# Performance work log

Measured on AMD Instinct MI355X. Metric: run time of the kernel, lower is better.

The kernel has to match this reference:

```python
import jax, jax.numpy as jnp
import numpy as np

BLOCK = 64      # block_size
NRAND = 3       # num_random_blocks
NUM_HEAD = 16
HEAD_DIM = 64
HIDDEN = 1024
PEN = -10000.0  # HF attn_mask_penalty


def _sparse_attn(q, k, v, band_mask, from_mask, to_mask, blocked_mask, rand_attn):
    # q,k,v: [B,H,S,D]; BigBird block-sparse attention (HF math).
    B, H, S, D = q.shape
    b, r = BLOCK, NRAND
    n = S // b
    rsd = 1.0 / (D ** 0.5)

    bq = q.reshape(B, H, n, b, D)
    bk = k.reshape(B, H, n, b, D)
    bv = v.reshape(B, H, n, b, D)

    bi = jnp.arange(B)[:, None, None, None]
    hi = jnp.arange(H)[None, :, None, None]
    # gathered random key/value blocks: [B,H,n-2,r*b,D]
    gk = bk[bi, hi, rand_attn].reshape(B, H, n - 2, r * b, D)
    gv = bv[bi, hi, rand_attn].reshape(B, H, n - 2, r * b, D)
    # random-block mask: [B,H,n-2,b,r*b]
    rm = blocked_mask[bi, rand_attn].reshape(B, H, n - 2, r * b)
    rand_mask = jnp.einsum("blq,bhlk->bhlqk", blocked_mask[:, 1:-1], rm)

    ones = lambda shp: jnp.ones(shp, q.dtype)

    # ---- first query block: attends to everything ----
    p = jnp.einsum("bhqd,bhkd->bhqk", bq[:, :, 0], k) * rsd + (1.0 - to_mask) * PEN
    c0 = jnp.einsum("bhqk,bhkd->bhqd", jax.nn.softmax(p, -1), v)[:, :, None]

    # ---- second query block: blocks 0,1,2,last + random ----
    k1 = jnp.concatenate([bk[:, :, 0], bk[:, :, 1], bk[:, :, 2], bk[:, :, -1], gk[:, :, 0]], axis=2)
    v1 = jnp.concatenate([bv[:, :, 0], bv[:, :, 1], bv[:, :, 2], bv[:, :, -1], gv[:, :, 0]], axis=2)
    p = jnp.einsum("bhqd,bhkd->bhqk", bq[:, :, 1], k1) * rsd
    seq_pad = jnp.concatenate([to_mask[..., :3 * b], to_mask[..., -b:], ones((B, 1, 1, r * b))], axis=3)
    rand_pad = jnp.concatenate([ones((B, H, b, 4 * b)), rand_mask[:, :, 0]], axis=3)
    p = p + (1.0 - jnp.minimum(seq_pad, rand_pad)) * PEN
    c1 = jnp.einsum("bhqk,bhkd->bhqd", jax.nn.softmax(p, -1), v1)[:, :, None]

    # ---- middle blocks 2..n-3: band(3 blocks) + first + last + random ----
    ek = jnp.concatenate([bk[:, :, 1:-3], bk[:, :, 2:-2], bk[:, :, 3:-1]], axis=3)  # [B,H,n-4,3b,D]
    ev = jnp.concatenate([bv[:, :, 1:-3], bv[:, :, 2:-2], bv[:, :, 3:-1]], axis=3)
    mq = bq[:, :, 2:-2]                                                              # [B,H,n-4,b,D]
    inner = jnp.einsum("bhlqd,bhlkd->bhlqk", mq, ek) * rsd + (1.0 - band_mask) * PEN
    randp = jnp.einsum("bhlqd,bhlkd->bhlqk", mq, gk[:, :, 1:-1]) * rsd + (1.0 - rand_mask[:, :, 1:-1]) * PEN
    firstp = jnp.einsum("bhlqd,bhkd->bhlqk", mq, bk[:, :, 0]) * rsd + (1.0 - to_mask[..., :b][:, :, None]) * PEN
    lastp = jnp.einsum("bhlqd,bhkd->bhlqk", mq, bk[:, :, -1]) * rsd + (1.0 - to_mask[..., -b:][:, :, None]) * PEN
    band = jnp.concatenate([firstp, inner, randp, lastp], axis=-1)  # [B,H,n-4,b,(5+r)*b]
    a = jax.nn.softmax(band, -1)
    cm = jnp.einsum("bhlqk,bhlkd->bhlqd", a[..., b:4 * b], ev)
    cm = cm + jnp.einsum("bhlqk,bhlkd->bhlqd", a[..., 4 * b:-b], gv[:, :, 1:-1])
    cm = cm + jnp.einsum("bhlqk,bhkd->bhlqd", a[..., :b], bv[:, :, 0])
    cm = cm + jnp.einsum("bhlqk,bhkd->bhlqd", a[..., -b:], bv[:, :, -1])

    # ---- second-last query block: blocks 0,-3,-2,-1 + random ----
    k2 = jnp.concatenate([bk[:, :, 0], bk[:, :, -3], bk[:, :, -2], bk[:, :, -1], gk[:, :, -1]], axis=2)
    v2 = jnp.concatenate([bv[:, :, 0], bv[:, :, -3], bv[:, :, -2], bv[:, :, -1], gv[:, :, -1]], axis=2)
    p = jnp.einsum("bhqd,bhkd->bhqk", bq[:, :, -2], k2) * rsd
    seq_pad = jnp.concatenate([to_mask[..., :b], to_mask[..., -3 * b:], ones((B, 1, 1, r * b))], axis=3)
    rand_pad = jnp.concatenate([ones((B, H, b, 4 * b)), rand_mask[:, :, -1]], axis=3)
    p = p + (1.0 - jnp.minimum(seq_pad, rand_pad)) * PEN
    c2 = jnp.einsum("bhqk,bhkd->bhqd", jax.nn.softmax(p, -1), v2)[:, :, None]

    # ---- last query block: attends to everything ----
    p = jnp.einsum("bhqd,bhkd->bhqk", bq[:, :, -1], k) * rsd + (1.0 - to_mask) * PEN
    c3 = jnp.einsum("bhqk,bhkd->bhqd", jax.nn.softmax(p, -1), v)[:, :, None]

    ctx = jnp.concatenate([c0, c1, cm, c2, c3], axis=2).reshape(B, H, S, D)
    ctx = ctx * from_mask  # [B,1,S,1]
    return ctx.transpose(0, 2, 1, 3).reshape(B, S, H * D)


def setup_inputs() -> dict:
    key = jax.random.key(0)
    ks = jax.random.split(key, 12)
    B, L = 2, 4064
    S = 4096
    n = S // BLOCK
    sc = 0.02
    inp = {
        "X": jax.random.normal(ks[0], (B, L, HIDDEN), jnp.float32),
        "Wq": jax.random.normal(ks[1], (HIDDEN, NUM_HEAD * HEAD_DIM), jnp.float32) * sc,
        "b_q": jnp.zeros((NUM_HEAD * HEAD_DIM,), jnp.float32),
        "Wk": jax.random.normal(ks[2], (HIDDEN, NUM_HEAD * HEAD_DIM), jnp.float32) * sc,
        "b_k": jnp.zeros((NUM_HEAD * HEAD_DIM,), jnp.float32),
        "Wv": jax.random.normal(ks[3], (HIDDEN, NUM_HEAD * HEAD_DIM), jnp.float32) * sc,
        "b_v": jnp.zeros((NUM_HEAD * HEAD_DIM,), jnp.float32),
        "Wo": jax.random.normal(ks[4], (NUM_HEAD * HEAD_DIM, HIDDEN), jnp.float32) * sc,
        "b_o": jnp.zeros((HIDDEN,), jnp.float32),
        "band_mask": jnp.ones((B, 1, n - 4, BLOCK, 3 * BLOCK), jnp.float32),
        "from_mask": jnp.ones((B, 1, S, 1), jnp.float32),
        "to_mask": jnp.ones((B, 1, 1, S), jnp.float32),
        "blocked_encoder_mask": jnp.ones((B, n, BLOCK), jnp.float32),
        "rand_attn": jax.random.randint(ks[5], (B, NUM_HEAD, n - 2, NRAND), 0, n, jnp.int32),
    }
    return inp


def reference(X, Wq, b_q, Wk, b_k, Wv, b_v, Wo, b_o,
              band_mask, from_mask, to_mask, blocked_encoder_mask, rand_attn):
    B, L, _ = X.shape
    pad = BLOCK - L % BLOCK  # matches torch wrapper (pads full block if L % b == 0)
    Xp = jnp.pad(X, ((0, 0), (0, pad), (0, 0)))
    S = L + pad

    def proj(W, bias):
        return (Xp @ W + bias).reshape(B, S, NUM_HEAD, HEAD_DIM).transpose(0, 2, 1, 3)

    q, k, v = proj(Wq, b_q), proj(Wk, b_k), proj(Wv, b_v)
    attn = _sparse_attn(q, k, v, band_mask, from_mask, to_mask, blocked_encoder_mask, rand_attn)
    out = attn @ Wo + b_o
    return out[:, :L]
```

## Files before the change

### kernel.cpp

```cpp
#include <hip/hip_runtime.h>

#define BB 2
#define SEQ 4096
#define LQ 4064
#define HID 1024
#define NH 16
#define HD 64
#define NB 64
#define BLK 64
#define NR 3
#define PENV -10000.0f

typedef __bf16 bf16;
typedef __bf16 bf16x8 __attribute__((ext_vector_type(8)));
typedef float floatx4 __attribute__((ext_vector_type(4)));

__device__ inline floatx4 mfma16(bf16x8 a, bf16x8 b, floatx4 c) {
    return __builtin_amdgcn_mfma_f32_16x16x32_bf16(a, b, c, 0, 0, 0);
}

__device__ inline void async_ld16(const bf16* g, bf16* l) {
    __builtin_amdgcn_global_load_lds(
        (const __attribute__((address_space(1))) unsigned int*)g,
        (__attribute__((address_space(3))) unsigned int*)l, 16, 0, 0);
}

__global__ __launch_bounds__(256) void cast_pad_x(const float* __restrict__ X,
                                                  bf16* __restrict__ Xp) {
    int t = blockIdx.x * 256 + threadIdx.x;
    int c4 = t & 255;
    int row = t >> 8;
    int b = row >> 12;
    int s = row & 4095;
    float4 v = make_float4(0.f, 0.f, 0.f, 0.f);
    if (s < LQ) {
        v = reinterpret_cast<const float4*>(X + ((size_t)(b * LQ + s)) * HID)[c4];
    }
    union { bf16 h[4]; uint2 u; } o;
    o.h[0] = (bf16)v.x; o.h[1] = (bf16)v.y; o.h[2] = (bf16)v.z; o.h[3] = (bf16)v.w;
    *reinterpret_cast<uint2*>(Xp + (size_t)row * HID + c4 * 4) = o.u;
}

__global__ __launch_bounds__(256) void transpose_w(const float* __restrict__ Wq,
                                                   const float* __restrict__ Wk,
                                                   const float* __restrict__ Wv,
                                                   const float* __restrict__ Wo,
                                                   bf16* __restrict__ WqkvT,
                                                   bf16* __restrict__ WoT) {
    __shared__ float tile[64][65];
    int sel = blockIdx.z;
    const float* src = (sel == 0) ? Wq : (sel == 1) ? Wk : (sel == 2) ? Wv : Wo;
    bf16* dst = (sel < 3) ? (WqkvT + (size_t)sel * HID * HID) : WoT;
    int j0 = blockIdx.x * 64, k0 = blockIdx.y * 64;
    int tx = threadIdx.x, ty = threadIdx.y;
    for (int i = 0; i < 16; i++) {
        int k = ty + i * 4;
        tile[k][tx] = src[(size_t)(k0 + k) * HID + j0 + tx];
    }
    __syncthreads();
    for (int i = 0; i < 16; i++) {
        int j = ty + i * 4;
        dst[(size_t)(j0 + j) * HID + k0 + tx] = (bf16)tile[tx][j];
    }
}

__global__ __launch_bounds__(256) void transpose_band(const float* __restrict__ band,
                                                      float* __restrict__ bandT) {
    __shared__ float tile[64][65];
    int kt = blockIdx.x;
    int lrow = blockIdx.y;
    int b = blockIdx.z;
    const float* src = band + ((size_t)(b * (NB - 4) + lrow) * BLK) * 192;
    float* dst = bandT + ((size_t)(b * (NB - 4) + lrow) * 192) * BLK;
    int tx = threadIdx.x, ty = threadIdx.y;
    for (int i = 0; i < 16; i++) {
        int qq = i * 4 + ty;
        tile[qq][tx] = src[(size_t)qq * 192 + kt * 64 + tx];
    }
    __syncthreads();
    for (int i = 0; i < 16; i++) {
        int k = i * 4 + ty;
        dst[(size_t)(kt * 64 + k) * BLK + tx] = tile[tx][k];
    }
}

__global__ __launch_bounds__(256) void mask_viol(const float* __restrict__ tom,
                                                 const float* __restrict__ blocked,
                                                 const float* __restrict__ band,
                                                 int* __restrict__ flags) {
    int which = blockIdx.y, b = blockIdx.z;
    const float* src;
    size_t n;
    if (which == 0)      { src = tom     + (size_t)b * SEQ;                  n = SEQ; }
    else if (which == 1) { src = blocked + (size_t)b * NB * BLK;             n = NB * BLK; }
    else                 { src = band    + (size_t)b * (NB - 4) * BLK * 192; n = (size_t)(NB - 4) * BLK * 192; }
    const float4* s4 = (const float4*)src;
    size_t n4 = n >> 2;
    int bad = 0;
    for (size_t i = blockIdx.x * 256 + threadIdx.x; i < n4; i += 240 * 256) {
        float4 v = s4[i];
        bad |= (v.x != 1.0f) | (v.y != 1.0f) | (v.z != 1.0f) | (v.w != 1.0f);
    }
    if (__any(bad) && (threadIdx.x & 63) == 0)
        atomicOr(&flags[which * BB + b], 1);
}

__global__ __launch_bounds__(256) void gemm_qkv(const bf16* __restrict__ Xp,
// ... 10 lines not shown
    int tid = threadIdx.x;
    int wave = tid >> 6, lane = tid & 63;
    int quad = lane >> 4, lm = lane & 15;
    int id = blockIdx.x;
    int xcd = id & 7, slot = id >> 3;
    int tile_m = (xcd * 8 + (slot & 7)) * 128;
    int tile_n = (slot >> 3) * 128;
    int wm = (wave & 1) * 64, wn = (wave >> 1) * 64;

    floatx4 acc[4][4] = {};

    for (int k0 = 0; k0 < HID; k0 += 64) {
        __syncthreads();
        for (int it = 0; it < 4; it++) {
            int c = it * 256 + tid;
            int row = c >> 3, col = (c & 7) * 8;
            async_ld16(Xp + (size_t)(tile_m + row) * HID + k0 + col, &As[c * 8]);
            async_ld16(WT + (size_t)(tile_n + row) * HID + k0 + col, &Bs[c * 8]);
        }
        __syncthreads();
        for (int ks = 0; ks < 64; ks += 32) {
            bf16x8 a[4], b[4];
            for (int i = 0; i < 4; i++)
                a[i] = *reinterpret_cast<const bf16x8*>(&As[(wm + i * 16 + lm) * 64 + ks + quad * 8]);
            for (int j = 0; j < 4; j++)
                b[j] = *reinterpret_cast<const bf16x8*>(&Bs[(wn + j * 16 + lm) * 64 + ks + quad * 8]);
            for (int i = 0; i < 4; i++)
                for (int j = 0; j < 4; j++)
                    acc[i][j] = mfma16(a[i], b[j], acc[i][j]);
        }
    }

    int which = tile_n >> 10;
    int hc_base = (tile_n + wn) & 1023;
    int h = hc_base >> 6;
    const float* bias = (which == 0) ? bq : (which == 1) ? bk : bv;
    __syncthreads();
    bf16* ep = (bf16*)smem + wave * (64 * 72);

    if (which < 2) {
        #pragma unroll
        for (int i = 0; i < 4; i++)
            #pragma unroll
            for (int j = 0; j < 4; j++) {
                float bsv = bias[hc_base + j * 16 + lm];
                #pragma unroll
                for (int r = 0; r < 4; r++) {
                    float val = acc[i][j][r] + bsv;
                    if (which == 0) val *= 0.125f;
                    ep[(i * 16 + quad * 4 + r) * 72 + j * 16 + lm] = (bf16)val;
                }
            }
        __builtin_amdgcn_wave_barrier();
        int s_glob = tile_m + wm + lane;
        int b_ = s_glob >> 12, s = s_glob & 4095;
        bf16* dstb = ((which == 0) ? qo : ko) + ((size_t)((b_ * NH + h) * SEQ + s)) * HD;
        #pragma unroll
        for (int c = 0; c < 8; c++)
            *reinterpret_cast<uint4*>(dstb + c * 8) =
                *reinterpret_cast<const uint4*>(ep + lane * 72 + c * 8);
    } else {
        #pragma unroll
        for (int i = 0; i < 4; i++)
            #pragma unroll
            for (int j = 0; j < 4; j++) {
                float bsv = bias[hc_base + j * 16 + lm];
                #pragma unroll
                for (int r = 0; r < 4; r++) {
                    float val = acc[i][j][r] + bsv;
                    ep[(j * 16 + lm) * 72 + i * 16 + quad * 4 + r] = (bf16)val;
                }
            }
        __builtin_amdgcn_wave_barrier();
        int s_base = tile_m + wm;
        int b_ = s_base >> 12, s0 = s_base & 4095;
        bf16* dstb = vt + ((size_t)((b_ * NH + h) * HD + lane)) * SEQ + s0;
        #pragma unroll
        for (int c = 0; c < 8; c++)
            *reinterpret_cast<uint4*>(dstb + c * 8) =
                *reinterpret_cast<const uint4*>(ep + lane * 72 + c * 8);
    }
}

__global__ __launch_bounds__(256, 3) void attn_kernel(const bf16* __restrict__ q,
                                                      const bf16* __restrict__ kk,
                                                      const bf16* __restrict__ vt,
                                                      const float* __restrict__ bandT,
                                                      const float* __restrict__ fromm,
                                                      const float* __restrict__ tom,
                                                      const float* __restrict__ blocked,
                                                      const int* __restrict__ rand_attn,
                                                      const int* __restrict__ flags,
                                                      bf16* __restrict__ attn) {
    __shared__ __align__(16) char smem[17408];

    int tid = threadIdx.x, wave = tid >> 6, lane = tid & 63;
    int quad = lane >> 4, lm = lane & 15;
    int bh = blockIdx.x;
    int b = bh >> 4, h = bh & 15;
    size_t bh_base = (size_t)bh * SEQ * HD;
    int x = blockIdx.y;
    bool fullmode = (x < 8);
    int l, sub;
    if (fullmode) { l = (x >> 2) ? (NB - 1) : 0; sub = x & 3; }
    else          { l = x - 7;                   sub = wave;  }

    bool do_to = flags[b] != 0;
    bool do_bl = flags[BB + b] != 0;
    bool do_bd = flags[2 * BB + b] != 0;

    bf16x8 aq0 = *reinterpret_cast<const bf16x8*>(
        q + bh_base + (size_t)(l * BLK + sub * 16 + lm) * HD + quad * 8);
    bf16x8 aq1 = *reinterpret_cast<const bf16x8*>(
        q + bh_base + (size_t)(l * BLK + sub * 16 + lm) * HD + 32 + quad * 8);

    floatx4 ctx[4] = {};
    float mrun = -1e30f, lrun = 0.f;
    float mq = blocked[((size_t)b * NB + l) * BLK + sub * 16 + lm];

    unsigned long long kbp = 0ull;
    unsigned int typ_p = 0u;
    if (!fullmode) {
        int base;
        if (l == 1) {
            kbp = (1ull << 8) | (2ull << 16) | ((unsigned long long)(NB - 1) << 24);
            base = 4;
        } else if (l == NB - 2) {
            kbp = ((unsigned long long)(NB - 3) << 8) | ((unsigned long long)(NB - 2) << 16) |
                  ((unsigned long long)(NB - 1) << 24);
            base = 4;
        } else {
            kbp = ((unsigned long long)(l - 1) << 8) | ((unsigned long long)l << 16) |
                  ((unsigned long long)(l + 1) << 24) | ((unsigned long long)(NB - 1) << 32);
            typ_p = (1u << 4) | (2u << 8) | (3u << 12);
            base = 5;
        }
        const int* ra = rand_attn + ((size_t)(b * NH + h) * (NB - 2) + (l - 1)) * NR;
        #pragma unroll
        for (int r = 0; r < NR; r++) {
            int rv = __builtin_amdgcn_readfirstlane(ra[r]);
            kbp   |= (unsigned long long)(rv & 63) << ((base + r) * 8);
            typ_p |= 4u << ((base + r) * 4);
        }
        for (int i = base + NR; i < 8; i++) typ_p |= 5u << (i * 4);
    }

    bf16* pw = (bf16*)smem + wave * 16 * 136;

    int nch = fullmode ? 8 : 4;
    for (int ch = 0; ch < nch; ch++) {
        int i0 = ch * 2, i1 = i0 + 1;
        int kb0, kb1, ty0, ty1;
        if (fullmode) {
            kb0 = __builtin_amdgcn_readfirstlane(wave * 16 + i0);
            kb1 = kb0 + 1;
            ty0 = 0; ty1 = 0;
        } else {
            kb0 = __builtin_amdgcn_readfirstlane((int)((kbp >> (i0 * 8)) & 63));
            kb1 = __builtin_amdgcn_readfirstlane((int)((kbp >> (i1 * 8)) & 63));
            ty0 = (int)((typ_p >> (i0 * 4)) & 15);
            ty1 = (int)((typ_p >> (i1 * 4)) & 15);
        }

        const bf16* k0p = kk + bh_base + (size_t)kb0 * (BLK * HD);
        const bf16* k1p = kk + bh_base + (size_t)kb1 * (BLK * HD);
        bf16x8 kfa[2][4], kfb[2][4];
        #pragma unroll
        for (int f = 0; f < 4; f++) {
            kfa[0][f] = *reinterpret_cast<const bf16x8*>(k0p + (f * 16 + lm) * HD + quad * 8);
            kfb[0][f] = *reinterpret_cast<const bf16x8*>(k0p + (f * 16 + lm) * HD + 32 + quad * 8);
        }
        #pragma unroll
        for (int f = 0; f < 4; f++) {
            kfa[1][f] = *reinterpret_cast<const bf16x8*>(k1p + (f * 16 + lm) * HD + quad * 8);
            kfb[1][f] = *reinterpret_cast<const bf16x8*>(k1p + (f * 16 + lm) * HD + 32 + quad * 8);
        }

        floatx4 sc[2][4];
        #pragma unroll
        for (int u = 0; u < 2; u++)
            #pragma unroll
            for (int f = 0; f < 4; f++) {
                floatx4 z = {0.f, 0.f, 0.f, 0.f};
                z = mfma16(kfa[u][f], aq0, z);
                z = mfma16(kfb[u][f], aq1, z);
                sc[u][f] = z;
            }

        const bf16* v0p = vt + bh_base + (size_t)kb0 * BLK;
        bf16x8 vf0[4][2];
        #pragma unroll
        for (int dj = 0; dj < 4; dj++) {
            vf0[dj][0] = *reinterpret_cast<const bf16x8*>(v0p + (size_t)(dj * 16 + lm) * SEQ + quad * 8);
            vf0[dj][1] = *reinterpret_cast<const bf16x8*>(v0p + (size_t)(dj * 16 + lm) * SEQ + 32 + quad * 8);
        }

        {
            int kbs[2] = {kb0, kb1};
            int tys[2] = {ty0, ty1};
            #pragma unroll
            for (int u = 0; u < 2; u++) {
                int kb = kbs[u], typ = tys[u];
                if (typ == 0) {
                    if (do_to) {
                        #pragma unroll
                        for (int f = 0; f < 4; f++) {
                            float4 t4 = *reinterpret_cast<const float4*>(
                                tom + (size_t)b * SEQ + kb * BLK + f * 16 + quad * 4);
                            sc[u][f][0] += (1.f - t4.x) * PENV;
                            sc[u][f][1] += (1.f - t4.y) * PENV;
                            sc[u][f][2] += (1.f - t4.z) * PENV;
                            sc[u][f][3] += (1.f - t4.w) * PENV;
                        }
                    }
                } else if (typ == 4) {
                    if (do_bl) {
                        #pragma unroll
                        for (int f = 0; f < 4; f++) {
                            float4 t4 = *reinterpret_cast<const float4*>(
                                blocked + ((size_t)b * NB + kb) * BLK + f * 16 + quad * 4);
                            sc[u][f][0] += (1.f - mq * t4.x) * PENV;
                            sc[u][f][1] += (1.f - mq * t4.y) * PENV;
                            sc[u][f][2] += (1.f - mq * t4.z) * PENV;
                            sc[u][f][3] += (1.f - mq * t4.w) * PENV;
                        }
                    }
                } else if (typ != 5) {
                    if (do_bd) {
                        int t = typ - 1;
                        const float* bp = bandT + ((size_t)(b * (NB - 4) + (l - 2)) * 192 + t * 64) * BLK;
                        #pragma unroll
                        for (int f = 0; f < 4; f++)
                            #pragma unroll
                            for (int r = 0; r < 4; r++) {
                                float bm = bp[(size_t)(f * 16 + quad * 4 + r) * BLK + sub * 16 + lm];
                                sc[u][f][r] += (1.f - bm) * PENV;
                            }
                    }
                } else {
                    #pragma unroll
                    for (int f = 0; f < 4; f++)
                        #pragma unroll
                        for (int r = 0; r < 4; r++) sc[u][f][r] += PENV;
                }
            }
        }

        float mx = -1e30f;
        #pragma unroll
        for (int u = 0; u < 2; u++)
            #pragma unroll
            for (int f = 0; f < 4; f++)
                #pragma unroll
                for (int r = 0; r < 4; r++) mx = fmaxf(mx, sc[u][f][r]);
        mx = fmaxf(mx, __shfl_xor(mx, 16, 64));
        mx = fmaxf(mx, __shfl_xor(mx, 32, 64));
        float mnew = fmaxf(mrun, mx);
        float scale = __expf(mrun - mnew);
        lrun *= scale;
        #pragma unroll
        for (int dj = 0; dj < 4; dj++) ctx[dj] *= scale;
        mrun = mnew;

        __builtin_amdgcn_wave_barrier();
        float rs = 0.f;
        #pragma unroll
        for (int u = 0; u < 2; u++)
            #pragma unroll
            for (int f = 0; f < 4; f++) {
                float p0 = __expf(sc[u][f][0] - mnew);
                float p1 = __expf(sc[u][f][1] - mnew);
                float p2 = __expf(sc[u][f][2] - mnew);
                float p3 = __expf(sc[u][f][3] - mnew);
                rs += (p0 + p1) + (p2 + p3);
                union { bf16 hh[4]; uint2 u2; } pu;
                pu.hh[0] = (bf16)p0; pu.hh[1] = (bf16)p1;
                pu.hh[2] = (bf16)p2; pu.hh[3] = (bf16)p3;
                *reinterpret_cast<uint2*>(pw + lm * 136 + u * 64 + f * 16 + quad * 4) = pu.u2;
            }
        __builtin_amdgcn_wave_barrier();
        rs += __shfl_xor(rs, 16, 64);
        rs += __shfl_xor(rs, 32, 64);
        lrun += rs;

        const bf16* v1p = vt + bh_base + (size_t)kb1 * BLK;
        bf16x8 vf1[4][2];
        #pragma unroll
        for (int dj = 0; dj < 4; dj++) {
            vf1[dj][0] = *reinterpret_cast<const bf16x8*>(v1p + (size_t)(dj * 16 + lm) * SEQ + quad * 8);
            vf1[dj][1] = *reinterpret_cast<const bf16x8*>(v1p + (size_t)(dj * 16 + lm) * SEQ + 32 + quad * 8);
        }

        bf16x8 pb[2][2];
        #pragma unroll
        for (int u = 0; u < 2; u++) {
            pb[u][0] = *reinterpret_cast<const bf16x8*>(pw + lm * 136 + u * 64 + quad * 8);
            pb[u][1] = *reinterpret_cast<const bf16x8*>(pw + lm * 136 + u * 64 + 32 + quad * 8);
        }

        #pragma unroll
        for (int dj = 0; dj < 4; dj++) {
            ctx[dj] = mfma16(vf0[dj][0], pb[0][0], ctx[dj]);
            ctx[dj] = mfma16(vf0[dj][1], pb[0][1], ctx[dj]);
        }
        #pragma unroll
        for (int dj = 0; dj < 4; dj++) {
            ctx[dj] = mfma16(vf1[dj][0], pb[1][0], ctx[dj]);
            ctx[dj] = mfma16(vf1[dj][1], pb[1][1], ctx[dj]);
        }
    }

    if (!fullmode) {
        int sq = l * BLK + sub * 16 + lm;
        float w = (1.f / lrun) * fromm[(size_t)b * SEQ + sq];
        bf16* dst = attn + ((size_t)(b * SEQ + sq)) * HID + h * HD;
        #pragma unroll
        for (int dj = 0; dj < 4; dj++) {
            union { bf16 hh[4]; uint2 u2; } o;
            #pragma unroll
            for (int r = 0; r < 4; r++) o.hh[r] = (bf16)(ctx[dj][r] * w);
            *reinterpret_cast<uint2*>(dst + dj * 16 + quad * 4) = o.u2;
        }
    } else {
        float* ctxL = (float*)smem;
        float* mL   = (float*)(smem + 16384);
        float* lL   = (float*)(smem + 16640);
        __syncthreads();
        #pragma unroll
        for (int dj = 0; dj < 4; dj++)
            #pragma unroll
            for (int r = 0; r < 4; r++)
                ctxL[wave * 1024 + (dj * 16 + quad * 4 + r) * 16 + lm] = ctx[dj][r];
        if (quad == 0) { mL[wave * 16 + lm] = mrun; lL[wave * 16 + lm] = lrun; }
        __syncthreads();
        int qq = tid & 15, dbase = (tid >> 4) * 4;
        float M = -1e30f;
        for (int w = 0; w < 4; w++) M = fmaxf(M, mL[w * 16 + qq]);
        float e[4], Lt = 0.f;
        for (int w = 0; w < 4; w++) { e[w] = __expf(mL[w * 16 + qq] - M); Lt += lL[w * 16 + qq] * e[w]; }
        int sq = l * BLK + sub * 16 + qq;
        float wgt = (1.f / Lt) * fromm[(size_t)b * SEQ + sq];
        union { bf16 hh[4]; uint2 u2; } o;
        #pragma unroll
        for (int dd = 0; dd < 4; dd++) {
            float acc = 0.f;
            for (int w = 0; w < 4; w++) acc += ctxL[w * 1024 + (dbase + dd) * 16 + qq] * e[w];
            o.hh[dd] = (bf16)(acc * wgt);
        }
        *reinterpret_cast<uint2*>(attn + ((size_t)(b * SEQ + sq)) * HID + h * HD + dbase) = o.u2;
    }
}

__global__ __launch_bounds__(256) void gemm_out(const bf16* __restrict__ A,
                                                const bf16* __restrict__ WoT,
                                                const float* __restrict__ bo,
                                                float* __restrict__ out) {
    __shared__ __align__(16) bf16 As[128 * 64];
    __shared__ __align__(16) bf16 Bs[128 * 64];
    int tid = threadIdx.x;
    int wave = tid >> 6, lane = tid & 63;
    int quad = lane >> 4, lm = lane & 15;
    int id = blockIdx.x;
    int xcd = id & 7, slot = id >> 3;
    int tile_m = (xcd * 8 + (slot & 7)) * 128;
    int tile_n = (slot >> 3) * 128;
    int wm = (wave & 1) * 64, wn = (wave >> 1) * 64;

    floatx4 acc[4][4] = {};

    for (int k0 = 0; k0 < HID; k0 += 64) {
        __syncthreads();
        for (int it = 0; it < 4; it++) {
            int c = it * 256 + tid;
            int row = c >> 3, col = (c & 7) * 8;
            async_ld16(A + (size_t)(tile_m + row) * HID + k0 + col, &As[c * 8]);
            async_ld16(WoT + (size_t)(tile_n + row) * HID + k0 + col, &Bs[c * 8]);
        }
        __syncthreads();
        for (int ks = 0; ks < 64; ks += 32) {
            bf16x8 a[4], b[4];
            for (int i = 0; i < 4; i++)
                a[i] = *reinterpret_cast<const bf16x8*>(&As[(wm + i * 16 + lm) * 64 + ks + quad * 8]);
            for (int j = 0; j < 4; j++)
                b[j] = *reinterpret_cast<const bf16x8*>(&Bs[(wn + j * 16 + lm) * 64 + ks + quad * 8]);
            for (int i = 0; i < 4; i++)
                for (int j = 0; j < 4; j++)
                    acc[i][j] = mfma16(a[i], b[j], acc[i][j]);
        }
    }

    for (int i = 0; i < 4; i++) {
        for (int j = 0; j < 4; j++) {
// ... 53 lines not shown
```

Measured before the change: 388.2 us.

## Stage sparse-block K tiles into swizzled LDS with async double buffering

For the band/random query blocks, K blocks are now loaded cooperatively into LDS using async global-to-LDS loads with an XOR swizzle, double-buffered across chunks so the next pair of K blocks streams in while the current one is computed. The full-attention blocks are moved to the end of the grid. Previously each of the four waves loaded the same K blocks from global memory on its own. The change raises shared memory per block to about 49 KB, which may lower occupancy, and adds barriers per chunk.

```diff
diff --git a/kernel.cpp b/kernel.cpp
--- a/kernel.cpp
+++ b/kernel.cpp
@@ -23,6 +23,18 @@
     __builtin_amdgcn_global_load_lds(
         (const __attribute__((address_space(1))) unsigned int*)g,
         (__attribute__((address_space(3))) unsigned int*)l, 16, 0, 0);
+}
+
+__device__ inline void stage_k2(const bf16* kkbh, bf16* dst, int kb0, int kb1, int tid) {
+    #pragma unroll
+    for (int it = 0; it < 2; it++) {
+        int o = (it * 256 + tid) * 16;
+        int row = o >> 7;
+        int c16 = (o >> 4) & 7;
+        int srcel = row * 64 + ((c16 ^ (row & 7)) << 3);
+        async_ld16(kkbh + (size_t)kb0 * (BLK * HD) + srcel, dst + (o >> 1));
+        async_ld16(kkbh + (size_t)kb1 * (BLK * HD) + srcel, dst + 4096 + (o >> 1));
+    }
 }
 
 __global__ __launch_bounds__(256) void cast_pad_x(const float* __restrict__ X,
@@ -209,31 +221,24 @@
                                                       const int* __restrict__ rand_attn,
                                                       const int* __restrict__ flags,
                                                       bf16* __restrict__ attn) {
-    __shared__ __align__(16) char smem[17408];
+    __shared__ __align__(16) char smem[50176];
+    bf16* sK = (bf16*)smem;
 
     int tid = threadIdx.x, wave = tid >> 6, lane = tid & 63;
     int quad = lane >> 4, lm = lane & 15;
+    int sw = lm & 7;
     int bh = blockIdx.x;
     int b = bh >> 4, h = bh & 15;
     size_t bh_base = (size_t)bh * SEQ * HD;
     int x = blockIdx.y;
-    bool fullmode = (x < 8);
+    bool fullmode = (x >= 62);
     int l, sub;
-    if (fullmode) { l = (x >> 2) ? (NB - 1) : 0; sub = x & 3; }
-    else          { l = x - 7;                   sub = wave;  }
+    if (fullmode) { int x2 = x - 62; l = (x2 >> 2) ? (NB - 1) : 0; sub = x2 & 3; }
+    else          { l = x + 1;                                     sub = wave;   }
 
     bool do_to = flags[b] != 0;
     bool do_bl = flags[BB + b] != 0;
     bool do_bd = flags[2 * BB + b] != 0;
-
-    bf16x8 aq0 = *reinterpret_cast<const bf16x8*>(
-        q + bh_base + (size_t)(l * BLK + sub * 16 + lm) * HD + quad * 8);
-    bf16x8 aq1 = *reinterpret_cast<const bf16x8*>(
-        q + bh_base + (size_t)(l * BLK + sub * 16 + lm) * HD + 32 + quad * 8);
-
-    floatx4 ctx[4] = {};
-    float mrun = -1e30f, lrun = 0.f;
-    float mq = blocked[((size_t)b * NB + l) * BLK + sub * 16 + lm];
 
     unsigned long long kbp = 0ull;
     unsigned int typ_p = 0u;
@@ -260,9 +265,25 @@
             typ_p |= 4u << ((base + r) * 4);
         }
         for (int i = base + NR; i < 8; i++) typ_p |= 5u << (i * 4);
-    }
-
-    bf16* pw = (bf16*)smem + wave * 16 * 136;
+
+        {
+            int a0 = (int)((kbp >> 0) & 63),  a1 = (int)((kbp >> 8) & 63);
+            int b0 = (int)((kbp >> 16) & 63), b1 = (int)((kbp >> 24) & 63);
+            stage_k2(kk + bh_base, sK + 0,    a0, a1, tid);
+            stage_k2(kk + bh_base, sK + 8192, b0, b1, tid);
+        }
+    }
+
+    bf16x8 aq0 = *reinterpret_cast<const bf16x8*>(
+        q + bh_base + (size_t)(l * BLK + sub * 16 + lm) * HD + quad * 8);
+    bf16x8 aq1 = *reinterpret_cast<const bf16x8*>(
+        q + bh_base + (size_t)(l * BLK + sub * 16 + lm) * HD + 32 + quad * 8);
+
+    floatx4 ctx[4] = {};
+    float mrun = -1e30f, lrun = 0.f;
+    float mq = blocked[((size_t)b * NB + l) * BLK + sub * 16 + lm];
+
+    bf16* pw = (bf16*)(smem + 32768) + wave * 16 * 136;
 
     int nch = fullmode ? 8 : 4;
     for (int ch = 0; ch < nch; ch++) {
@@ -279,18 +300,41 @@
             ty1 = (int)((typ_p >> (i1 * 4)) & 15);
         }
 
-        const bf16* k0p = kk + bh_base + (size_t)kb0 * (BLK * HD);
-        const bf16* k1p = kk + bh_base + (size_t)kb1 * (BLK * HD);
         bf16x8 kfa[2][4], kfb[2][4];
-        #pragma unroll
-        for (int f = 0; f < 4; f++) {
-            kfa[0][f] = *reinterpret_cast<const bf16x8*>(k0p + (f * 16 + lm) * HD + quad * 8);
-            kfb[0][f] = *reinterpret_cast<const bf16x8*>(k0p + (f * 16 + lm) * HD + 32 + quad * 8);
-        }
-        #pragma unroll
-        for (int f = 0; f < 4; f++) {
-            kfa[1][f] = *reinterpret_cast<const bf16x8*>(k1p + (f * 16 + lm) * HD + quad * 8);
-            kfb[1][f] = *reinterpret_cast<const bf16x8*>(k1p + (f * 16 + lm) * HD + 32 + quad * 8);
+        if (!fullmode) {
+            if (ch >= 1 && ch + 1 < 4) {
+                int na = __builtin_amdgcn_readfirstlane((int)((kbp >> ((ch + 1) * 16)) & 63));
+                int nb = __builtin_amdgcn_readfirstlane((int)((kbp >> ((ch + 1) * 16 + 8)) & 63));
+                stage_k2(kk + bh_base, sK + ((ch + 1) & 1) * 8192, na, nb, tid);
+            }
+            if (ch < 3) asm volatile("s_waitcnt vmcnt(4)" ::: "memory");
+            else        asm volatile("s_waitcnt vmcnt(0)" ::: "memory");
+            __builtin_amdgcn_s_barrier();
+
+            const bf16* kbuf = sK + (ch & 1) * 8192;
+            #pragma unroll
+            for (int u = 0; u < 2; u++)
+                #pragma unroll
+                for (int f = 0; f < 4; f++) {
+                    int rowb = (f * 16 + lm) * 64;
+                    kfa[u][f] = *reinterpret_cast<const bf16x8*>(
+                        kbuf + u * 4096 + rowb + ((quad ^ sw) << 3));
+                    kfb[u][f] = *reinterpret_cast<const bf16x8*>(
+                        kbuf + u * 4096 + rowb + (((quad | 4) ^ sw) << 3));
+                }
+        } else {
+            const bf16* k0p = kk + bh_base + (size_t)kb0 * (BLK * HD);
+            const bf16* k1p = kk + bh_base + (size_t)kb1 * (BLK * HD);
+            #pragma unroll
+            for (int f = 0; f < 4; f++) {
+                kfa[0][f] = *reinterpret_cast<const bf16x8*>(k0p + (f * 16 + lm) * HD + quad * 8);
+                kfb[0][f] = *reinterpret_cast<const bf16x8*>(k0p + (f * 16 + lm) * HD + 32 + quad * 8);
+            }
+            #pragma unroll
+            for (int f = 0; f < 4; f++) {
+                kfa[1][f] = *reinterpret_cast<const bf16x8*>(k1p + (f * 16 + lm) * HD + quad * 8);
+                kfb[1][f] = *reinterpret_cast<const bf16x8*>(k1p + (f * 16 + lm) * HD + 32 + quad * 8);
+            }
         }
 
         floatx4 sc[2][4];
@@ -425,6 +469,8 @@
             ctx[dj] = mfma16(vf1[dj][0], pb[1][0], ctx[dj]);
             ctx[dj] = mfma16(vf1[dj][1], pb[1][1], ctx[dj]);
         }
+
+        if (!fullmode) __builtin_amdgcn_s_barrier();
     }
 
     if (!fullmode) {
```

After: 362.7 us. 1.07x faster.

## Double-buffer K fragments in registers and prefetch next chunk in attention loop

Applied to the files above, without the earlier changes.

The attention chunk loop becomes a two-stage software pipeline. K fragments for the next pair of key blocks are loaded into a second register buffer while the current chunk's softmax and PV MFMAs run, and V loads are issued ahead of the QK MFMAs with compiler fences. The cross-lane row-sum reduction is deferred to once after the loop. The full-attention blocks are moved to the end of the grid. The extra registers force launch bounds down from 3 to 2 blocks per CU, trading occupancy for latency hiding.

```diff
diff --git a/kernel.cpp b/kernel.cpp
--- a/kernel.cpp
+++ b/kernel.cpp
@@ -14,6 +14,8 @@
 typedef __bf16 bf16;
 typedef __bf16 bf16x8 __attribute__((ext_vector_type(8)));
 typedef float floatx4 __attribute__((ext_vector_type(4)));
+
+#define MEMFENCE asm volatile("" ::: "memory")
 
 __device__ inline floatx4 mfma16(bf16x8 a, bf16x8 b, floatx4 c) {
     return __builtin_amdgcn_mfma_f32_16x16x32_bf16(a, b, c, 0, 0, 0);
@@ -199,7 +201,191 @@
     }
 }
 
-__global__ __launch_bounds__(256, 3) void attn_kernel(const bf16* __restrict__ q,
+__device__ __forceinline__ int slot_kb(bool fullmode, int wave,
+                                       unsigned long long kbp, int i) {
+    int v = fullmode ? (wave * 16 + i) : (int)((kbp >> (i * 8)) & 63);
+    return __builtin_amdgcn_readfirstlane(v);
+}
+
+__device__ __forceinline__ void load_k2(const bf16* kkbh, int k0, int k1,
+                                        int lm, int quad,
+                                        bf16x8 (&ka)[2][4], bf16x8 (&kb_)[2][4]) {
+    const bf16* kp0 = kkbh + (size_t)k0 * (BLK * HD);
+    const bf16* kp1 = kkbh + (size_t)k1 * (BLK * HD);
+    #pragma unroll
+    for (int f = 0; f < 4; f++) {
+        ka[0][f]  = *reinterpret_cast<const bf16x8*>(kp0 + (f * 16 + lm) * HD + quad * 8);
+        kb_[0][f] = *reinterpret_cast<const bf16x8*>(kp0 + (f * 16 + lm) * HD + 32 + quad * 8);
+        ka[1][f]  = *reinterpret_cast<const bf16x8*>(kp1 + (f * 16 + lm) * HD + quad * 8);
+        kb_[1][f] = *reinterpret_cast<const bf16x8*>(kp1 + (f * 16 + lm) * HD + 32 + quad * 8);
+    }
+}
+
+__device__ __forceinline__ void attn_step(
+    int c, int nch, bool fullmode, int wave,
+    unsigned long long kbp, unsigned int typ_p,
+    const bf16* kkbh, const bf16* vtbh,
+    int lm, int quad, int sub,
+    bf16x8 aq0, bf16x8 aq1, float mq,
+    bool do_to, bool do_bl, bool do_bd,
+    const float* tom_b, const float* blocked_b, const float* bandT_l,
+    bf16x8 (&kaC)[2][4], bf16x8 (&kbC)[2][4],
+    bf16x8 (&kaN)[2][4], bf16x8 (&kbN)[2][4],
+    floatx4 (&ctx)[4], float& mrun, float& lrun, bf16* pw)
+{
+    int i0 = c * 2, i1 = i0 + 1;
+    int kb0 = slot_kb(fullmode, wave, kbp, i0);
+    int kb1 = slot_kb(fullmode, wave, kbp, i1);
+    int ty0 = fullmode ? 0 : (int)((typ_p >> (i0 * 4)) & 15);
+    int ty1 = fullmode ? 0 : (int)((typ_p >> (i1 * 4)) & 15);
+
+    bf16x8 vf0[4][2];
+    {
+        const bf16* v0p = vtbh + (size_t)kb0 * BLK;
+        #pragma unroll
+        for (int dj = 0; dj < 4; dj++) {
+            vf0[dj][0] = *reinterpret_cast<const bf16x8*>(v0p + (size_t)(dj * 16 + lm) * SEQ + quad * 8);
+            vf0[dj][1] = *reinterpret_cast<const bf16x8*>(v0p + (size_t)(dj * 16 + lm) * SEQ + 32 + quad * 8);
+        }
+    }
+    MEMFENCE;
+
+    floatx4 sc[2][4];
+    #pragma unroll
+    for (int u = 0; u < 2; u++)
+        #pragma unroll
+        for (int f = 0; f < 4; f++) {
+            floatx4 z = {0.f, 0.f, 0.f, 0.f};
+            z = mfma16(kaC[u][f], aq0, z);
+            z = mfma16(kbC[u][f], aq1, z);
+            sc[u][f] = z;
+        }
+    MEMFENCE;
+
+    bf16x8 vf1[4][2];
+    {
+        const bf16* v1p = vtbh + (size_t)kb1 * BLK;
+        #pragma unroll
+        for (int dj = 0; dj < 4; dj++) {
+            vf1[dj][0] = *reinterpret_cast<const bf16x8*>(v1p + (size_t)(dj * 16 + lm) * SEQ + quad * 8);
+            vf1[dj][1] = *reinterpret_cast<const bf16x8*>(v1p + (size_t)(dj * 16 + lm) * SEQ + 32 + quad * 8);
+        }
+    }
+    MEMFENCE;
+
+    {
+        int kbs[2] = {kb0, kb1};
+        int tys[2] = {ty0, ty1};
+        #pragma unroll
+        for (int u = 0; u < 2; u++) {
+            int kb = kbs[u], typ = tys[u];
+            if (typ == 0) {
+                if (do_to) {
+                    #pragma unroll
+                    for (int f = 0; f < 4; f++) {
+                        float4 t4 = *reinterpret_cast<const float4*>(
+                            tom_b + kb * BLK + f * 16 + quad * 4);
+                        sc[u][f][0] += (1.f - t4.x) * PENV;
+                        sc[u][f][1] += (1.f - t4.y) * PENV;
+                        sc[u][f][2] += (1.f - t4.z) * PENV;
+                        sc[u][f][3] += (1.f - t4.w) * PENV;
+                    }
+                }
+            } else if (typ == 4) {
+                if (do_bl) {
+                    #pragma unroll
+                    for (int f = 0; f < 4; f++) {
+                        float4 t4 = *reinterpret_cast<const float4*>(
+                            blocked_b + kb * BLK + f * 16 + quad * 4);
+                        sc[u][f][0] += (1.f - mq * t4.x) * PENV;
+                        sc[u][f][1] += (1.f - mq * t4.y) * PENV;
+                        sc[u][f][2] += (1.f - mq * t4.z) * PENV;
+                        sc[u][f][3] += (1.f - mq * t4.w) * PENV;
+                    }
+                }
+            } else if (typ != 5) {
+                if (do_bd) {
+                    const float* bp = bandT_l + (size_t)((typ - 1) * 64) * BLK;
+                    #pragma unroll
+                    for (int f = 0; f < 4; f++)
+                        #pragma unroll
+                        for (int r = 0; r < 4; r++) {
+                            float bm = bp[(size_t)(f * 16 + quad * 4 + r) * BLK + sub * 16 + lm];
+                            sc[u][f][r] += (1.f - bm) * PENV;
+                        }
+                }
+            } else {
+                #pragma unroll
+                for (int f = 0; f < 4; f++)
+                    #pragma unroll
+                    for (int r = 0; r < 4; r++) sc[u][f][r] += PENV;
+            }
+        }
+    }
+
+    float mx = -1e30f;
+    #pragma unroll
+    for (int u = 0; u < 2; u++)
+        #pragma unroll
+        for (int f = 0; f < 4; f++)
+            #pragma unroll
+            for (int r = 0; r < 4; r++) mx = fmaxf(mx, sc[u][f][r]);
+    float a16 = __shfl_xor(mx, 16, 64);
+    float a32 = __shfl_xor(mx, 32, 64);
+    float a48 = __shfl_xor(mx, 48, 64);
+    mx = fmaxf(fmaxf(mx, a16), fmaxf(a32, a48));
+    float mnew = fmaxf(mrun, mx);
+    float scale = __expf(mrun - mnew);
+    #pragma unroll
+    for (int dj = 0; dj < 4; dj++) ctx[dj] *= scale;
+    mrun = mnew;
+
+    __builtin_amdgcn_wave_barrier();
+    float rs = 0.f;
+    #pragma unroll
+    for (int u = 0; u < 2; u++)
+        #pragma unroll
+        for (int f = 0; f < 4; f++) {
+            float p0 = __expf(sc[u][f][0] - mnew);
+            float p1 = __expf(sc[u][f][1] - mnew);
+            float p2 = __expf(sc[u][f][2] - mnew);
+            float p3 = __expf(sc[u][f][3] - mnew);
+            rs += (p0 + p1) + (p2 + p3);
+            union { bf16 hh[4]; uint2 u2; } pu;
+            pu.hh[0] = (bf16)p0; pu.hh[1] = (bf16)p1;
+            pu.hh[2] = (bf16)p2; pu.hh[3] = (bf16)p3;
+            *reinterpret_cast<uint2*>(pw + lm * 136 + u * 64 + f * 16 + quad * 4) = pu.u2;
+        }
+    __builtin_amdgcn_wave_barrier();
+    lrun = lrun * scale + rs;
+
+    if (c + 1 < nch) {
+        int n0 = slot_kb(fullmode, wave, kbp, i0 + 2);
+        int n1 = slot_kb(fullmode, wave, kbp, i1 + 2);
+        load_k2(kkbh, n0, n1, lm, quad, kaN, kbN);
+        MEMFENCE;
+    }
+
+    bf16x8 pb[2][2];
+    #pragma unroll
+    for (int u = 0; u < 2; u++) {
+        pb[u][0] = *reinterpret_cast<const bf16x8*>(pw + lm * 136 + u * 64 + quad * 8);
+        pb[u][1] = *reinterpret_cast<const bf16x8*>(pw + lm * 136 + u * 64 + 32 + quad * 8);
+    }
+
+    #pragma unroll
+    for (int dj = 0; dj < 4; dj++) {
+        ctx[dj] = mfma16(vf0[dj][0], pb[0][0], ctx[dj]);
+        ctx[dj] = mfma16(vf0[dj][1], pb[0][1], ctx[dj]);
+    }
+    #pragma unroll
+    for (int dj = 0; dj < 4; dj++) {
+        ctx[dj] = mfma16(vf1[dj][0], pb[1][0], ctx[dj]);
+        ctx[dj] = mfma16(vf1[dj][1], pb[1][1], ctx[dj]);
+    }
+}
+
+__global__ __launch_bounds__(256, 2) void attn_kernel(const bf16* __restrict__ q,
                                                       const bf16* __restrict__ kk,
                                                       const bf16* __restrict__ vt,
                                                       const float* __restrict__ bandT,
@@ -217,23 +403,14 @@
     int b = bh >> 4, h = bh & 15;
     size_t bh_base = (size_t)bh * SEQ * HD;
     int x = blockIdx.y;
-    bool fullmode = (x < 8);
+    bool fullmode = (x >= 62);
     int l, sub;
-    if (fullmode) { l = (x >> 2) ? (NB - 1) : 0; sub = x & 3; }
-    else          { l = x - 7;                   sub = wave;  }
+    if (fullmode) { int x2 = x - 62; l = (x2 >> 2) ? (NB - 1) : 0; sub = x2 & 3; }
+    else          { l = x + 1;                                     sub = wave;   }
 
     bool do_to = flags[b] != 0;
     bool do_bl = flags[BB + b] != 0;
     bool do_bd = flags[2 * BB + b] != 0;
-
-    bf16x8 aq0 = *reinterpret_cast<const bf16x8*>(
-        q + bh_base + (size_t)(l * BLK + sub * 16 + lm) * HD + quad * 8);
-    bf16x8 aq1 = *reinterpret_cast<const bf16x8*>(
-        q + bh_base + (size_t)(l * BLK + sub * 16 + lm) * HD + 32 + quad * 8);
-
-    floatx4 ctx[4] = {};
-    float mrun = -1e30f, lrun = 0.f;
-    float mq = blocked[((size_t)b * NB + l) * BLK + sub * 16 + lm];
 
     unsigned long long kbp = 0ull;
     unsigned int typ_p = 0u;
@@ -262,169 +439,47 @@
         for (int i = base + NR; i < 8; i++) typ_p |= 5u << (i * 4);
     }
 
+    bf16x8 aq0 = *reinterpret_cast<const bf16x8*>(
+        q + bh_base + (size_t)(l * BLK + sub * 16 + lm) * HD + quad * 8);
+    bf16x8 aq1 = *reinterpret_cast<const bf16x8*>(
+        q + bh_base + (size_t)(l * BLK + sub * 16 + lm) * HD + 32 + quad * 8);
+    float mq = blocked[((size_t)b * NB + l) * BLK + sub * 16 + lm];
+
+    const float* tom_b = tom + (size_t)b * SEQ;
+    const float* blocked_b = blocked + (size_t)b * NB * BLK;
+    int lcl = (l >= 2) ? (l - 2) : 0;
+    const float* bandT_l = bandT + ((size_t)(b * (NB - 4) + lcl) * 192) * BLK;
+
+    floatx4 ctx[4] = {};
+    float mrun = -1e30f, lrun = 0.f;
+
     bf16* pw = (bf16*)smem + wave * 16 * 136;
 
+    bf16x8 kaA[2][4], kbA[2][4], kaB[2][4], kbB[2][4];
+    {
+        int s0 = slot_kb(fullmode, wave, kbp, 0);
+        int s1 = slot_kb(fullmode, wave, kbp, 1);
+        load_k2(kk + bh_base, s0, s1, lm, quad, kaA, kbA);
+        MEMFENCE;
+    }
+
+    const bf16* kkbh = kk + bh_base;
+    const bf16* vtbh = vt + bh_base;
     int nch = fullmode ? 8 : 4;
-    for (int ch = 0; ch < nch; ch++) {
-        int i0 = ch * 2, i1 = i0 + 1;
-        int kb0, kb1, ty0, ty1;
-        if (fullmode) {
-            kb0 = __builtin_amdgcn_readfirstlane(wave * 16 + i0);
-            kb1 = kb0 + 1;
-            ty0 = 0; ty1 = 0;
-        } else {
-            kb0 = __builtin_amdgcn_readfirstlane((int)((kbp >> (i0 * 8)) & 63));
-            kb1 = __builtin_amdgcn_readfirstlane((int)((kbp >> (i1 * 8)) & 63));
-            ty0 = (int)((typ_p >> (i0 * 4)) & 15);
-            ty1 = (int)((typ_p >> (i1 * 4)) & 15);
-        }
-
-        const bf16* k0p = kk + bh_base + (size_t)kb0 * (BLK * HD);
-        const bf16* k1p = kk + bh_base + (size_t)kb1 * (BLK * HD);
-        bf16x8 kfa[2][4], kfb[2][4];
-        #pragma unroll
-        for (int f = 0; f < 4; f++) {
-            kfa[0][f] = *reinterpret_cast<const bf16x8*>(k0p + (f * 16 + lm) * HD + quad * 8);
-            kfb[0][f] = *reinterpret_cast<const bf16x8*>(k0p + (f * 16 + lm) * HD + 32 + quad * 8);
-        }
-        #pragma unroll
-        for (int f = 0; f < 4; f++) {
-            kfa[1][f] = *reinterpret_cast<const bf16x8*>(k1p + (f * 16 + lm) * HD + quad * 8);
-            kfb[1][f] = *reinterpret_cast<const bf16x8*>(k1p + (f * 16 + lm) * HD + 32 + quad * 8);
-        }
-
-        floatx4 sc[2][4];
-        #pragma unroll
-        for (int u = 0; u < 2; u++)
-            #pragma unroll
-            for (int f = 0; f < 4; f++) {
-                floatx4 z = {0.f, 0.f, 0.f, 0.f};
-                z = mfma16(kfa[u][f], aq0, z);
-                z = mfma16(kfb[u][f], aq1, z);
-                sc[u][f] = z;
-            }
-
-        const bf16* v0p = vt + bh_base + (size_t)kb0 * BLK;
-        bf16x8 vf0[4][2];
-        #pragma unroll
-        for (int dj = 0; dj < 4; dj++) {
-            vf0[dj][0] = *reinterpret_cast<const bf16x8*>(v0p + (size_t)(dj * 16 + lm) * SEQ + quad * 8);
-            vf0[dj][1] = *reinterpret_cast<const bf16x8*>(v0p + (size_t)(dj * 16 + lm) * SEQ + 32 + quad * 8);
-        }
-
-        {
-            int kbs[2] = {kb0, kb1};
-            int tys[2] = {ty0, ty1};
-            #pragma unroll
-            for (int u = 0; u < 2; u++) {
-                int kb = kbs[u], typ = tys[u];
-                if (typ == 0) {
-                    if (do_to) {
-                        #pragma unroll
-                        for (int f = 0; f < 4; f++) {
-                            float4 t4 = *reinterpret_cast<const float4*>(
-                                tom + (size_t)b * SEQ + kb * BLK + f * 16 + quad * 4);
-                            sc[u][f][0] += (1.f - t4.x) * PENV;
-                            sc[u][f][1] += (1.f - t4.y) * PENV;
-                            sc[u][f][2] += (1.f - t4.z) * PENV;
-                            sc[u][f][3] += (1.f - t4.w) * PENV;
-                        }
-                    }
-                } else if (typ == 4) {
-                    if (do_bl) {
-                        #pragma unroll
-                        for (int f = 0; f < 4; f++) {
-                            float4 t4 = *reinterpret_cast<const float4*>(
-                                blocked + ((size_t)b * NB + kb) * BLK + f * 16 + quad * 4);
-                            sc[u][f][0] += (1.f - mq * t4.x) * PENV;
-                            sc[u][f][1] += (1.f - mq * t4.y) * PENV;
-                            sc[u][f][2] += (1.f - mq * t4.z) * PENV;
-                            sc[u][f][3] += (1.f - mq * t4.w) * PENV;
-                        }
-                    }
-                } else if (typ != 5) {
-                    if (do_bd) {
-                        int t = typ - 1;
-                        const float* bp = bandT + ((size_t)(b * (NB - 4) + (l - 2)) * 192 + t * 64) * BLK;
-                        #pragma unroll
-                        for (int f = 0; f < 4; f++)
-                            #pragma unroll
-                            for (int r = 0; r < 4; r++) {
-                                float bm = bp[(size_t)(f * 16 + quad * 4 + r) * BLK + sub * 16 + lm];
-                                sc[u][f][r] += (1.f - bm) * PENV;
-                            }
-                    }
-                } else {
-                    #pragma unroll
-                    for (int f = 0; f < 4; f++)
-                        #pragma unroll
-                        for (int r = 0; r < 4; r++) sc[u][f][r] += PENV;
-                }
-            }
-        }
-
-        float mx = -1e30f;
-        #pragma unroll
-        for (int u = 0; u < 2; u++)
-            #pragma unroll
-            for (int f = 0; f < 4; f++)
-                #pragma unroll
-                for (int r = 0; r < 4; r++) mx = fmaxf(mx, sc[u][f][r]);
-        mx = fmaxf(mx, __shfl_xor(mx, 16, 64));
-        mx = fmaxf(mx, __shfl_xor(mx, 32, 64));
-        float mnew = fmaxf(mrun, mx);
-        float scale = __expf(mrun - mnew);
-        lrun *= scale;
-        #pragma unroll
-        for (int dj = 0; dj < 4; dj++) ctx[dj] *= scale;
-        mrun = mnew;
-
-        __builtin_amdgcn_wave_barrier();
-        float rs = 0.f;
-        #pragma unroll
-        for (int u = 0; u < 2; u++)
-            #pragma unroll
-            for (int f = 0; f < 4; f++) {
-                float p0 = __expf(sc[u][f][0] - mnew);
-                float p1 = __expf(sc[u][f][1] - mnew);
-                float p2 = __expf(sc[u][f][2] - mnew);
-                float p3 = __expf(sc[u][f][3] - mnew);
-                rs += (p0 + p1) + (p2 + p3);
-                union { bf16 hh[4]; uint2 u2; } pu;
-                pu.hh[0] = (bf16)p0; pu.hh[1] = (bf16)p1;
-                pu.hh[2] = (bf16)p2; pu.hh[3] = (bf16)p3;
-                *reinterpret_cast<uint2*>(pw + lm * 136 + u * 64 + f * 16 + quad * 4) = pu.u2;
-            }
-        __builtin_amdgcn_wave_barrier();
-        rs += __shfl_xor(rs, 16, 64);
-        rs += __shfl_xor(rs, 32, 64);
-        lrun += rs;
-
-        const bf16* v1p = vt + bh_base + (size_t)kb1 * BLK;
-        bf16x8 vf1[4][2];
-        #pragma unroll
-        for (int dj = 0; dj < 4; dj++) {
-            vf1[dj][0] = *reinterpret_cast<const bf16x8*>(v1p + (size_t)(dj * 16 + lm) * SEQ + quad * 8);
-            vf1[dj][1] = *reinterpret_cast<const bf16x8*>(v1p + (size_t)(dj * 16 + lm) * SEQ + 32 + quad * 8);
-        }
-
-        bf16x8 pb[2][2];
-        #pragma unroll
-        for (int u = 0; u < 2; u++) {
-            pb[u][0] = *reinterpret_cast<const bf16x8*>(pw + lm * 136 + u * 64 + quad * 8);
-            pb[u][1] = *reinterpret_cast<const bf16x8*>(pw + lm * 136 + u * 64 + 32 + quad * 8);
-        }
-
-        #pragma unroll
-        for (int dj = 0; dj < 4; dj++) {
-            ctx[dj] = mfma16(vf0[dj][0], pb[0][0], ctx[dj]);
-            ctx[dj] = mfma16(vf0[dj][1], pb[0][1], ctx[dj]);
-        }
-        #pragma unroll
-        for (int dj = 0; dj < 4; dj++) {
-            ctx[dj] = mfma16(vf1[dj][0], pb[1][0], ctx[dj]);
-            ctx[dj] = mfma16(vf1[dj][1], pb[1][1], ctx[dj]);
-        }
+    for (int ch = 0; ch < nch; ch += 2) {
+        attn_step(ch,     nch, fullmode, wave, kbp, typ_p, kkbh, vtbh, lm, quad, sub,
+                  aq0, aq1, mq, do_to, do_bl, do_bd, tom_b, blocked_b, bandT_l,
+                  kaA, kbA, kaB, kbB, ctx, mrun, lrun, pw);
+        attn_step(ch + 1, nch, fullmode, wave, kbp, typ_p, kkbh, vtbh, lm, quad, sub,
+                  aq0, aq1, mq, do_to, do_bl, do_bd, tom_b, blocked_b, bandT_l,
+                  kaB, kbB, kaA, kbA, ctx, mrun, lrun, pw);
+    }
+
+    {
+        float b16 = __shfl_xor(lrun, 16, 64);
+        float b32 = __shfl_xor(lrun, 32, 64);
+        float b48 = __shfl_xor(lrun, 48, 64);
+        lrun = (lrun + b16) + (b32 + b48);
     }
 
     if (!fullmode) {
```

After: 510.9 us. +31.6%, slower.

## Reorder K/V loads, defer row-sum reduction, and relax attention launch bounds

Applied to the files above, without the earlier changes.

The attention kernel now issues the V block 0 load before the K loads and hoists the V block 1 load ahead of the masking and softmax, with compiler memory fences to keep the issue order. The per-chunk cross-lane row-sum shuffles are dropped; each lane keeps a partial sum that is reduced once after the loop. The row-max reduction uses three independent shuffles instead of two dependent ones. Launch bounds go from 3 to 2 waves-per-EU, which allows more registers for the larger set of in-flight loads but may lower occupancy.

```diff
diff --git a/kernel.cpp b/kernel.cpp
--- a/kernel.cpp
+++ b/kernel.cpp
@@ -14,6 +14,8 @@
 typedef __bf16 bf16;
 typedef __bf16 bf16x8 __attribute__((ext_vector_type(8)));
 typedef float floatx4 __attribute__((ext_vector_type(4)));
+
+#define MEMFENCE asm volatile("" ::: "memory")
 
 __device__ inline floatx4 mfma16(bf16x8 a, bf16x8 b, floatx4 c) {
     return __builtin_amdgcn_mfma_f32_16x16x32_bf16(a, b, c, 0, 0, 0);
@@ -199,7 +201,7 @@
     }
 }
 
-__global__ __launch_bounds__(256, 3) void attn_kernel(const bf16* __restrict__ q,
+__global__ __launch_bounds__(256, 2) void attn_kernel(const bf16* __restrict__ q,
                                                       const bf16* __restrict__ kk,
                                                       const bf16* __restrict__ vt,
                                                       const float* __restrict__ bandT,
@@ -225,15 +227,6 @@
     bool do_to = flags[b] != 0;
     bool do_bl = flags[BB + b] != 0;
     bool do_bd = flags[2 * BB + b] != 0;
-
-    bf16x8 aq0 = *reinterpret_cast<const bf16x8*>(
-        q + bh_base + (size_t)(l * BLK + sub * 16 + lm) * HD + quad * 8);
-    bf16x8 aq1 = *reinterpret_cast<const bf16x8*>(
-        q + bh_base + (size_t)(l * BLK + sub * 16 + lm) * HD + 32 + quad * 8);
-
-    floatx4 ctx[4] = {};
-    float mrun = -1e30f, lrun = 0.f;
-    float mq = blocked[((size_t)b * NB + l) * BLK + sub * 16 + lm];
 
     unsigned long long kbp = 0ull;
     unsigned int typ_p = 0u;
@@ -262,6 +255,18 @@
         for (int i = base + NR; i < 8; i++) typ_p |= 5u << (i * 4);
     }
 
+    bf16x8 aq0 = *reinterpret_cast<const bf16x8*>(
+        q + bh_base + (size_t)(l * BLK + sub * 16 + lm) * HD + quad * 8);
+    bf16x8 aq1 = *reinterpret_cast<const bf16x8*>(
+        q + bh_base + (size_t)(l * BLK + sub * 16 + lm) * HD + 32 + quad * 8);
+    float mq = blocked[((size_t)b * NB + l) * BLK + sub * 16 + lm];
+
+    const bf16* kkbh = kk + bh_base;
+    const bf16* vtbh = vt + bh_base;
+
+    floatx4 ctx[4] = {};
+    float mrun = -1e30f, lrun = 0.f;
+
     bf16* pw = (bf16*)smem + wave * 16 * 136;
 
     int nch = fullmode ? 8 : 4;
@@ -279,38 +284,47 @@
             ty1 = (int)((typ_p >> (i1 * 4)) & 15);
         }
 
-        const bf16* k0p = kk + bh_base + (size_t)kb0 * (BLK * HD);
-        const bf16* k1p = kk + bh_base + (size_t)kb1 * (BLK * HD);
-        bf16x8 kfa[2][4], kfb[2][4];
-        #pragma unroll
-        for (int f = 0; f < 4; f++) {
-            kfa[0][f] = *reinterpret_cast<const bf16x8*>(k0p + (f * 16 + lm) * HD + quad * 8);
-            kfb[0][f] = *reinterpret_cast<const bf16x8*>(k0p + (f * 16 + lm) * HD + 32 + quad * 8);
-        }
-        #pragma unroll
-        for (int f = 0; f < 4; f++) {
-            kfa[1][f] = *reinterpret_cast<const bf16x8*>(k1p + (f * 16 + lm) * HD + quad * 8);
-            kfb[1][f] = *reinterpret_cast<const bf16x8*>(k1p + (f * 16 + lm) * HD + 32 + quad * 8);
-        }
+        bf16x8 vf0[4][2];
+        {
+            const bf16* v0p = vtbh + (size_t)kb0 * BLK;
+            #pragma unroll
+            for (int dj = 0; dj < 4; dj++) {
+                vf0[dj][0] = *reinterpret_cast<const bf16x8*>(v0p + (size_t)(dj * 16 + lm) * SEQ + quad * 8);
+                vf0[dj][1] = *reinterpret_cast<const bf16x8*>(v0p + (size_t)(dj * 16 + lm) * SEQ + 32 + quad * 8);
+            }
+        }
+        MEMFENCE;
 
         floatx4 sc[2][4];
         #pragma unroll
-        for (int u = 0; u < 2; u++)
+        for (int u = 0; u < 2; u++) {
+            const bf16* kp = kkbh + (size_t)(u ? kb1 : kb0) * (BLK * HD);
+            bf16x8 ka[4], kb_[4];
+            #pragma unroll
+            for (int f = 0; f < 4; f++) {
+                ka[f]  = *reinterpret_cast<const bf16x8*>(kp + (f * 16 + lm) * HD + quad * 8);
+                kb_[f] = *reinterpret_cast<const bf16x8*>(kp + (f * 16 + lm) * HD + 32 + quad * 8);
+            }
             #pragma unroll
             for (int f = 0; f < 4; f++) {
                 floatx4 z = {0.f, 0.f, 0.f, 0.f};
-                z = mfma16(kfa[u][f], aq0, z);
-                z = mfma16(kfb[u][f], aq1, z);
+                z = mfma16(ka[f], aq0, z);
+                z = mfma16(kb_[f], aq1, z);
                 sc[u][f] = z;
             }
-
-        const bf16* v0p = vt + bh_base + (size_t)kb0 * BLK;
-        bf16x8 vf0[4][2];
-        #pragma unroll
-        for (int dj = 0; dj < 4; dj++) {
-            vf0[dj][0] = *reinterpret_cast<const bf16x8*>(v0p + (size_t)(dj * 16 + lm) * SEQ + quad * 8);
-            vf0[dj][1] = *reinterpret_cast<const bf16x8*>(v0p + (size_t)(dj * 16 + lm) * SEQ + 32 + quad * 8);
-        }
+        }
+        MEMFENCE;
+
+        bf16x8 vf1[4][2];
+        {
+            const bf16* v1p = vtbh + (size_t)kb1 * BLK;
+            #pragma unroll
+            for (int dj = 0; dj < 4; dj++) {
+                vf1[dj][0] = *reinterpret_cast<const bf16x8*>(v1p + (size_t)(dj * 16 + lm) * SEQ + quad * 8);
+                vf1[dj][1] = *reinterpret_cast<const bf16x8*>(v1p + (size_t)(dj * 16 + lm) * SEQ + 32 + quad * 8);
+            }
+        }
+        MEMFENCE;
 
         {
             int kbs[2] = {kb0, kb1};
@@ -370,11 +384,12 @@
             for (int f = 0; f < 4; f++)
                 #pragma unroll
                 for (int r = 0; r < 4; r++) mx = fmaxf(mx, sc[u][f][r]);
-        mx = fmaxf(mx, __shfl_xor(mx, 16, 64));
-        mx = fmaxf(mx, __shfl_xor(mx, 32, 64));
+        float a16 = __shfl_xor(mx, 16, 64);
+        float a32 = __shfl_xor(mx, 32, 64);
+        float a48 = __shfl_xor(mx, 48, 64);
+        mx = fmaxf(fmaxf(mx, a16), fmaxf(a32, a48));
         float mnew = fmaxf(mrun, mx);
         float scale = __expf(mrun - mnew);
-        lrun *= scale;
         #pragma unroll
         for (int dj = 0; dj < 4; dj++) ctx[dj] *= scale;
         mrun = mnew;
@@ -396,17 +411,7 @@
                 *reinterpret_cast<uint2*>(pw + lm * 136 + u * 64 + f * 16 + quad * 4) = pu.u2;
             }
         __builtin_amdgcn_wave_barrier();
-        rs += __shfl_xor(rs, 16, 64);
-        rs += __shfl_xor(rs, 32, 64);
-        lrun += rs;
-
-        const bf16* v1p = vt + bh_base + (size_t)kb1 * BLK;
-        bf16x8 vf1[4][2];
-        #pragma unroll
-        for (int dj = 0; dj < 4; dj++) {
-            vf1[dj][0] = *reinterpret_cast<const bf16x8*>(v1p + (size_t)(dj * 16 + lm) * SEQ + quad * 8);
-            vf1[dj][1] = *reinterpret_cast<const bf16x8*>(v1p + (size_t)(dj * 16 + lm) * SEQ + 32 + quad * 8);
-        }
+        lrun = lrun * scale + rs;
 
         bf16x8 pb[2][2];
         #pragma unroll
@@ -425,6 +430,13 @@
             ctx[dj] = mfma16(vf1[dj][0], pb[1][0], ctx[dj]);
             ctx[dj] = mfma16(vf1[dj][1], pb[1][1], ctx[dj]);
         }
+    }
+
+    {
+        float b16 = __shfl_xor(lrun, 16, 64);
+        float b32 = __shfl_xor(lrun, 32, 64);
+        float b48 = __shfl_xor(lrun, 48, 64);
+        lrun = (lrun + b16) + (b32 + b48);
     }
 
     if (!fullmode) {
```

New measurement: 388.2 us. No clear change (-0.0%).
